# Kernel tuning notes

Hardware: AMD Instinct MI355X
Metric: run time of the kernel (lower is better)

The kernel has to match this reference:

```python
import jax, jax.numpy as jnp
import numpy as np
from jax import lax

B, T, J, C = 256, 512, 25, 3
IN_DIM = J * C  # 75
H = 256


def gru_layer(x, W_ih, W_hh, b_ih, b_hh):
    """PyTorch-semantics GRU layer. x: [B,T,Din] -> (out [B,T,H], h_T [B,H]).
    Gate order in stacked weights: r, z, n (PyTorch convention)."""
    Hh = W_hh.shape[1]
    # precompute input contributions for all timesteps
    xg = jnp.einsum('bti,gi->btg', x, W_ih) + b_ih  # [B,T,3H]

    def step(h, xg_t):
        hg = h @ W_hh.T + b_hh  # [B,3H]
        xr, xz, xn = jnp.split(xg_t, 3, axis=-1)
        hr, hz, hn = jnp.split(hg, 3, axis=-1)
        r = jax.nn.sigmoid(xr + hr)
        z = jax.nn.sigmoid(xz + hz)
        n = jnp.tanh(xn + r * hn)
        h_new = (1.0 - z) * n + z * h
        return h_new, h_new

    h0 = jnp.zeros((x.shape[0], Hh), x.dtype)
    hT, outs = lax.scan(step, h0, jnp.swapaxes(xg, 0, 1))  # scan over time
    return jnp.swapaxes(outs, 0, 1), hT


def setup_inputs() -> dict:
    key = jax.random.key(0)
    ks = jax.random.split(key, 12)
    s_in = 1.0 / np.sqrt(H)

    def u(k, shape):
        return jax.random.uniform(k, shape, jnp.float32, -s_in, s_in)

    return {
        'x': jax.random.normal(ks[0], (B, T, J, C), jnp.float32),
        'W_ih0': u(ks[1], (3 * H, IN_DIM)),
        'W_hh0': u(ks[2], (3 * H, H)),
        'b_ih0': u(ks[3], (3 * H,)),
        'b_hh0': u(ks[4], (3 * H,)),
        'W_ih1': u(ks[5], (3 * H, H)),
        'W_hh1': u(ks[6], (3 * H, H)),
        'b_ih1': u(ks[7], (3 * H,)),
        'b_hh1': u(ks[8], (3 * H,)),
        'fc_W': u(ks[9], (H, H)),
        'fc_b': u(ks[10], (H,)),
    }


def reference(x, W_ih0, W_hh0, b_ih0, b_hh0, W_ih1, W_hh1, b_ih1, b_hh1, fc_W, fc_b):
    b, t, j, c = x.shape
    xf = x.reshape(b, t, j * 3)  # matches torch view(B, T, J*3)
    out0, _ = gru_layer(xf, W_ih0, W_hh0, b_ih0, b_hh0)
    _, hT = gru_layer(out0, W_ih1, W_hh1, b_ih1, b_hh1)
    # unidirectional: final hidden state of last layer -> fc
    embedding = hT @ fc_W.T + fc_b  # [B, H]
    return embedding
```

## Files before the change

kernel.cpp:

```cpp
#include <hip/hip_runtime.h>
#include <hip/hip_bf16.h>
#include <stdint.h>
#include <stddef.h>


typedef _Float16 f16;
typedef _Float16 f16x8 __attribute__((ext_vector_type(8)));
typedef _Float16 f16x4 __attribute__((ext_vector_type(4)));
typedef float    f32x4 __attribute__((ext_vector_type(4)));

#define B_      256
#define T_      512
#define H_      256
#define G_      768
#define IN_RAW  75
#define KX      96
#define MROWS   (T_*B_)

__device__ __forceinline__ float sigm(float x){ return 1.f/(1.f+__expf(-x)); }
__device__ __forceinline__ float tanh_(float x){ return 1.f - 2.f/(1.f+__expf(2.f*x)); }

__global__ __launch_bounds__(256) void cast_x(const float* __restrict__ x,
                                              f16* __restrict__ xb){
  int idx = blockIdx.x*256 + threadIdx.x;
  int row = idx / KX;
  int j   = idx - row*KX;
  int t   = row >> 8;
  int b   = row & 255;
  float v = (j < IN_RAW) ? x[((size_t)b*T_ + t)*IN_RAW + j] : 0.f;
  xb[idx] = (f16)v;
}

__global__ __launch_bounds__(256) void cast_w(
    const float* __restrict__ Wih0, const float* __restrict__ Whh0,
    const float* __restrict__ Wih1, const float* __restrict__ Whh1,
    const float* __restrict__ fcW,
    const float* __restrict__ bih0, const float* __restrict__ bhh0,
    const float* __restrict__ bih1, const float* __restrict__ bhh1,
    f16* __restrict__ W0h, f16* __restrict__ Whh0h, f16* __restrict__ Wih1h,
    f16* __restrict__ Whh1h, f16* __restrict__ fcWh,
    float* __restrict__ bias0, float* __restrict__ bias1){
  int i = blockIdx.x*256 + threadIdx.x;
  if (i < 73728){ int r = i/KX, j = i - r*KX;
    W0h[i] = (f16)((j < IN_RAW) ? Wih0[r*IN_RAW + j] : 0.f); return; }
  i -= 73728;
  if (i < 196608){ Whh0h[i] = (f16)Whh0[i]; return; } i -= 196608;
  if (i < 196608){ Wih1h[i] = (f16)Wih1[i]; return; } i -= 196608;
  if (i < 196608){ Whh1h[i] = (f16)Whh1[i]; return; } i -= 196608;
  if (i < 65536){ fcWh[i] = (f16)fcW[i]; return; } i -= 65536;
  if (i < 768){ bias0[i] = bih0[i] + (i < 512 ? bhh0[i] : 0.f); return; } i -= 768;
  if (i < 768){ bias1[i] = bih1[i] + (i < 512 ? bhh1[i] : 0.f); }
}

__global__ __launch_bounds__(256) void cast_h(const float* __restrict__ hs,
                                              f16* __restrict__ hT){
  int i = blockIdx.x*256 + threadIdx.x;
  hT[i] = (f16)hs[i];
}

template<int K, int BN, bool OUTF32>
__global__ __launch_bounds__(256, 2) void gemm_k(const f16* __restrict__ A,
    const f16* __restrict__ W, const float* __restrict__ bias,
    void* __restrict__ outp, const int N){
  constexpr int NT = BN/16;
  const int tid  = threadIdx.x;
  const int wave = tid >> 6, lane = tid & 63;
  const int quad = lane >> 4, l16 = lane & 15;
  const long mbase = (long)blockIdx.x*128 + wave*32;
  const int  nbase = blockIdx.y*BN;
  f32x4 acc[2][NT] = {};
#pragma unroll 2
  for (int kc = 0; kc < K/32; ++kc){
    f16x8 a0 = *(const f16x8*)(A + (mbase +      l16)*K + kc*32 + quad*8);
    f16x8 a1 = *(const f16x8*)(A + (mbase + 16 + l16)*K + kc*32 + quad*8);
#pragma unroll
    for (int nt = 0; nt < NT; ++nt){
      f16x8 b = *(const f16x8*)(W + (long)(nbase + nt*16 + l16)*K + kc*32 + quad*8);
      acc[0][nt] = __builtin_amdgcn_mfma_f32_16x16x32_f16(a0, b, acc[0][nt], 0, 0, 0);
      acc[1][nt] = __builtin_amdgcn_mfma_f32_16x16x32_f16(a1, b, acc[1][nt], 0, 0, 0);
    }
  }
#pragma unroll
  for (int nt = 0; nt < NT; ++nt){
    const int col = nbase + nt*16 + l16;
    const float bv = bias[col];
#pragma unroll
    for (int af = 0; af < 2; ++af){
#pragma unroll
      for (int r = 0; r < 4; ++r){
        const long row = mbase + af*16 + quad*4 + r;
        float v = acc[af][nt][r] + bv;
        if (OUTF32) ((float*)outp)[row*(long)N + col] = v;
        else        ((f16*)outp)[row*(long)N + col] = (f16)v;
      }
    }
  }
}

template<int K>
__device__ __forceinline__ void gemm_body(const f16* __restrict__ A,
    const f16* __restrict__ W, const float* __restrict__ bias,
    f16* __restrict__ out, const int bx, const int by){
  const int tid  = threadIdx.x;
  const int wave = tid >> 6, lane = tid & 63;
  const int quad = lane >> 4, l16 = lane & 15;
  const int nbase = by*192;
#pragma unroll
  for (int mt = 0; mt < 2; ++mt){
    const long mbase = (long)bx*512 + mt*256 + wave*32;
    f32x4 acc[2][12] = {};
#pragma unroll 2
    for (int kc = 0; kc < K/32; ++kc){
      f16x8 a0 = *(const f16x8*)(A + (mbase +      l16)*K + kc*32 + quad*8);
      f16x8 a1 = *(const f16x8*)(A + (mbase + 16 + l16)*K + kc*32 + quad*8);
#pragma unroll
      for (int nt = 0; nt < 12; ++nt){
        f16x8 b = *(const f16x8*)(W + (long)(nbase + nt*16 + l16)*K + kc*32 + quad*8);
        acc[0][nt] = __builtin_amdgcn_mfma_f32_16x16x32_f16(a0, b, acc[0][nt], 0, 0, 0);
        acc[1][nt] = __builtin_amdgcn_mfma_f32_16x16x32_f16(a1, b, acc[1][nt], 0, 0, 0);
      }
    }
#pragma unroll
    for (int nt = 0; nt < 12; ++nt){
      const int col = nbase + nt*16 + l16;
      const float bv = bias[col];
#pragma unroll
      for (int af = 0; af < 2; ++af)
#pragma unroll
        for (int r = 0; r < 4; ++r)
          out[(mbase + af*16 + quad*4 + r)*(long)G_ + col] = (f16)(acc[af][nt][r] + bv);
    }
  }
}

__device__ __forceinline__ void scan_body(const f16* __restrict__ xg,
    const f16* __restrict__ Whh, const float* __restrict__ bhh,
    float* __restrict__ hstate, f16* __restrict__ out0,
    const int TC, const int bx){
  __shared__ f16   hbuf[2][16*264];
  __shared__ f16   nlds[32768];
  __shared__ float bnlds[256];
  const int tid  = threadIdx.x;
  const int wave = tid >> 6, lane = tid & 63;
  const int quad = lane >> 4, l16 = lane & 15;
  const int b0   = bx*16;
  const int jj   = wave*32 + quad*4;

  f16x8 w[2][2][8];
  f16x8 wn[2][4];
#pragma unroll
  for (int s = 0; s < 2; ++s){
#pragma unroll
    for (int g = 0; g < 2; ++g)
#pragma unroll
      for (int kc = 0; kc < 8; ++kc)
        w[s][g][kc] = *(const f16x8*)(Whh + (size_t)(g*256 + wave*32 + s*16 + l16)*H_ + kc*32 + quad*8);
#pragma unroll
    for (int kc = 0; kc < 4; ++kc)
      wn[s][kc] = *(const f16x8*)(Whh + (size_t)(512 + wave*32 + s*16 + l16)*H_ + kc*32 + quad*8);
  }
#pragma unroll
  for (int s = 0; s < 2; ++s){
#pragma unroll
    for (int g = 0; g < 2; ++g)
#pragma unroll
      for (int kc = 0; kc < 8; ++kc)
        asm volatile("" : "+v"(w[s][g][kc]));
#pragma unroll
    for (int kc = 0; kc < 4; ++kc)
      asm volatile("" : "+v"(wn[s][kc]));
  }

#pragma unroll
  for (int i = 0; i < 8; ++i){
    const int p  = tid*8 + i;
    const int f  = p >> 6, L = p & 63;
    const int wv = f >> 3, ss = (f >> 2) & 1, kcm = f & 3;
    const int row = 512 + wv*32 + ss*16 + (L & 15);
    const int k   = (kcm + 4)*32 + (L >> 4)*8;
    *(f16x8*)&nlds[p*8] = *(const f16x8*)(Whh + (size_t)row*H_ + k);
  }
  if (tid < 256) bnlds[tid] = bhh[512 + tid];

  f32x4 h[2];
#pragma unroll
  for (int s = 0; s < 2; ++s){
    h[s] = *(const f32x4*)(hstate + (size_t)(b0 + l16)*H_ + jj + s*16);
    f16x4 hh;
#pragma unroll
    for (int r = 0; r < 4; ++r) hh[r] = (f16)h[s][r];
    *(f16x4*)&hbuf[0][l16*264 + jj + s*16] = hh;
  }

  const f16* xgl = xg + (size_t)(b0 + l16)*G_ + jj;
  f16x4 cur[6];
#pragma unroll
  for (int s = 0; s < 2; ++s)
#pragma unroll
    for (int g = 0; g < 3; ++g)
      cur[s*3+g] = *(const f16x4*)(xgl + g*256 + s*16);

  __syncthreads();

  for (int t = 0; t < TC; ++t){
    const int pb = t & 1;
    f32x4 acc[2][3] = {};
#pragma unroll
    for (int kc = 0; kc < 8; ++kc){
      f16x8 hf = *(const f16x8*)(&hbuf[pb][l16*264 + kc*32 + quad*8]);
#pragma unroll
      for (int s = 0; s < 2; ++s){
        acc[s][0] = __builtin_amdgcn_mfma_f32_16x16x32_f16(w[s][0][kc], hf, acc[s][0], 0,0,0);
        acc[s][1] = __builtin_amdgcn_mfma_f32_16x16x32_f16(w[s][1][kc], hf, acc[s][1], 0,0,0);
        f16x8 wnf;
        if (kc < 4) wnf = wn[s][kc];
        else        wnf = *(const f16x8*)&nlds[(((wave*2+s)*4 + (kc-4))*64 + lane)*8];
        acc[s][2] = __builtin_amdgcn_mfma_f32_16x16x32_f16(wnf, hf, acc[s][2], 0,0,0);
      }
    }
    f16x4 hh[2];
#pragma unroll
    for (int s = 0; s < 2; ++s){
      const f32x4 bnv = *(const f32x4*)&bnlds[jj + s*16];
#pragma unroll
      for (int r = 0; r < 4; ++r){
        float rg = sigm((float)cur[s*3+0][r] + acc[s][0][r]);
        float zg = sigm((float)cur[s*3+1][r] + acc[s][1][r]);
        float ng = tanh_((float)cur[s*3+2][r] + rg*(acc[s][2][r] + bnv[r]));
        float hv = (1.f - zg)*ng + zg*h[s][r];
        h[s][r] = hv;
        hh[s][r] = (f16)hv;
      }
    }
    if (t+1 < TC){
      const f16* xn_ = xgl + (size_t)(t+1)*(B_*G_);
#pragma unroll
      for (int s = 0; s < 2; ++s)
#pragma unroll
        for (int g = 0; g < 3; ++g)
          cur[s*3+g] = *(const f16x4*)(xn_ + g*256 + s*16);
    }
#pragma unroll
    for (int s = 0; s < 2; ++s){
      *(f16x4*)&hbuf[pb^1][l16*264 + jj + s*16] = hh[s];
      if (out0)
        *(f16x4*)(out0 + ((size_t)t*B_ + b0 + l16)*H_ + jj + s*16) = hh[s];
    }
    __syncthreads();
  }

#pragma unroll
  for (int s = 0; s < 2; ++s)
    *(f32x4*)(hstate + (size_t)(b0 + l16)*H_ + jj + s*16) = h[s];
}

__global__ __launch_bounds__(512, 2) void fused(
    const f16* __restrict__ xg0, const f16* __restrict__ Whh0,
    const float* __restrict__ bhh0, float* __restrict__ h0s,
    f16* __restrict__ out0w,
    const f16* __restrict__ xg1, const f16* __restrict__ Whh1,
    const float* __restrict__ bhh1, float* __restrict__ h1s,
    const f16* __restrict__ g0A, const f16* __restrict__ g0W,
    const float* __restrict__ g0b, f16* __restrict__ g0out,
    const f16* __restrict__ g1A, const f16* __restrict__ g1W,
    const float* __restrict__ g1b, f16* __restrict__ g1out,
    const int TC, const int mask){
  const int bid = blockIdx.x;
  if (bid < 16){
    if (!(mask & 1)) return;
    scan_body(xg0, Whh0, bhh0, h0s, out0w, TC, bid);
  } else if (bid < 32){
    if (!(mask & 2)) return;
    scan_body(xg1, Whh1, bhh1, h1s, (f16*)nullptr, TC, bid - 16);
  } else {
    int g = bid - 32;
    const int half = TC/2;
    if (g < 2*TC){
      if (!(mask & 4)) return;
      gemm_body<96>(g0A, g0W, g0b, g0out, g % half, g / half);
    } else {
      g -= 2*TC;
      if (!(mask & 8)) return;
      gemm_body<256>(g1A, g1W, g1b, g1out, g % half, g / half);
    }
  }
}

extern "C" void kernel_launch(void* const* d_in, const int* in_sizes, int n_in,
                              void* d_out, int out_size, void* d_ws, size_t ws_size,
                              hipStream_t stream){
  (void)in_sizes; (void)n_in; (void)out_size;
  const float* x    = (const float*)d_in[0];
  const float* Wih0 = (const float*)d_in[1];
  const float* Whh0 = (const float*)d_in[2];
  const float* bih0 = (const float*)d_in[3];
  const float* bhh0 = (const float*)d_in[4];
  const float* Wih1 = (const float*)d_in[5];
  const float* Whh1 = (const float*)d_in[6];
  const float* bih1 = (const float*)d_in[7];
  const float* bhh1 = (const float*)d_in[8];
  const float* fcW  = (const float*)d_in[9];
  const float* fcb  = (const float*)d_in[10];

  char* ws = (char*)d_ws;
  size_t off = 0;
  auto alloc = [&](size_t bytes) -> void* {
    void* p = ws + off; off += (bytes + 255) & ~(size_t)255; return p;
  };
  f16*   xb    = (f16*)  alloc((size_t)MROWS*KX*2);
  f16*   W0h   = (f16*)  alloc((size_t)G_*KX*2);
  f16*   Whh0h = (f16*)  alloc((size_t)G_*H_*2);
  f16*   Wih1h = (f16*)  alloc((size_t)G_*H_*2);
  f16*   Whh1h = (f16*)  alloc((size_t)G_*H_*2);
  f16*   fcWh  = (f16*)  alloc((size_t)H_*H_*2);
  float* bias0 = (float*)alloc(G_*4);
  float* bias1 = (float*)alloc(G_*4);
  float* h0s   = (float*)alloc((size_t)B_*H_*4);
  float* h1s   = (float*)alloc((size_t)B_*H_*4);
  f16*   hTh   = (f16*)  alloc((size_t)B_*H_*2);
  const size_t fixed = off;

  int TC = 32;
  while (TC > 8 && fixed + (size_t)TC*1835008 + 1024 > ws_size) TC >>= 1;
  f16* xg0[2], *xg1[2], *out0[2];
  xg0[0]  = (f16*)alloc((size_t)TC*B_*G_*2);
  xg0[1]  = (f16*)alloc((size_t)TC*B_*G_*2);
  xg1[0]  = (f16*)alloc((size_t)TC*B_*G_*2);
  xg1[1]  = (f16*)alloc((size_t)TC*B_*G_*2);
  out0[0] = (f16*)alloc((size_t)TC*B_*H_*2);
  out0[1] = (f16*)alloc((size_t)TC*B_*H_*2);
  const int nc = T_ / TC;

  hipMemsetAsync(h0s, 0, (size_t)B_*H_*4*2, stream);
  hipLaunchKernelGGL(cast_x, dim3(49152), dim3(256), 0, stream, x, xb);
  hipLaunchKernelGGL(cast_w, dim3(2854), dim3(256), 0, stream,
                     Wih0, Whh0, Wih1, Whh1, fcW, bih0, bhh0, bih1, bhh1,
                     W0h, Whh0h, Wih1h, Whh1h, fcWh, bias0, bias1);

  hipLaunchKernelGGL((gemm_k<96,192,false>), dim3(TC*2,4), dim3(256), 0, stream,
                     xb, W0h, bias0, (void*)xg0[0], G_);

  const dim3 grid(32 + 4*TC);
  for (int i = 0; i <= nc + 1; ++i){
    int mask = 0;
    if (i < nc)            mask |= 1;
    if (i >= 2)            mask |= 2;
    if (i + 1 < nc)        mask |= 4;
    if (i >= 1 && i <= nc) mask |= 8;
    hipLaunchKernelGGL(fused, grid, dim3(512), 0, stream,
                       xg0[i&1], Whh0h, bhh0, h0s, out0[i&1],
                       xg1[i&1], Whh1h, bhh1, h1s,
                       xb + (size_t)(i+1)*TC*B_*KX, W0h, bias0, xg0[(i+1)&1],
                       out0[(i+1)&1], Wih1h, bias1, xg1[(i+1)&1],
                       TC, mask);
  }

  hipLaunchKernelGGL(cast_h, dim3(256), dim3(256), 0, stream, h1s, hTh);
  hipLaunchKernelGGL((gemm_k<256,64,true>), dim3(2,4), dim3(256), 0, stream,
                     hTh, fcWh, fcb, d_out, H_);
}
```

Baseline: 1.956 ms.

## Move full n-gate weights to LDS, swizzle h buffer, narrow fused GEMM tiles

The scan now keeps the whole n-gate recurrent weight slice in LDS (128KB) instead of half in registers, and pins the r/z weights in AGPRs. The hidden-state LDS buffer uses an XOR-swizzled layout in place of padding, meant to avoid bank conflicts on the per-step reads. The fused GEMM blocks drop from 192 to 128 output columns, and the grid grows to keep the same coverage with more, smaller blocks. This trades register pressure for more LDS traffic on every timestep and a larger LDS footprint per block.

Measured after the change: 1.917 ms. -2.0%, faster.

```diff
diff --git a/kernel.cpp b/kernel.cpp
--- a/kernel.cpp
+++ b/kernel.cpp
@@ -98,30 +98,30 @@
 }
 
 template<int K>
-__device__ __forceinline__ void gemm_body(const f16* __restrict__ A,
+__device__ __forceinline__ void gemm_body128(const f16* __restrict__ A,
     const f16* __restrict__ W, const float* __restrict__ bias,
     f16* __restrict__ out, const int bx, const int by){
   const int tid  = threadIdx.x;
   const int wave = tid >> 6, lane = tid & 63;
   const int quad = lane >> 4, l16 = lane & 15;
-  const int nbase = by*192;
+  const int nbase = by*128;
 #pragma unroll
   for (int mt = 0; mt < 2; ++mt){
     const long mbase = (long)bx*512 + mt*256 + wave*32;
-    f32x4 acc[2][12] = {};
+    f32x4 acc[2][8] = {};
 #pragma unroll 2
     for (int kc = 0; kc < K/32; ++kc){
       f16x8 a0 = *(const f16x8*)(A + (mbase +      l16)*K + kc*32 + quad*8);
       f16x8 a1 = *(const f16x8*)(A + (mbase + 16 + l16)*K + kc*32 + quad*8);
 #pragma unroll
-      for (int nt = 0; nt < 12; ++nt){
+      for (int nt = 0; nt < 8; ++nt){
         f16x8 b = *(const f16x8*)(W + (long)(nbase + nt*16 + l16)*K + kc*32 + quad*8);
         acc[0][nt] = __builtin_amdgcn_mfma_f32_16x16x32_f16(a0, b, acc[0][nt], 0, 0, 0);
         acc[1][nt] = __builtin_amdgcn_mfma_f32_16x16x32_f16(a1, b, acc[1][nt], 0, 0, 0);
       }
     }
 #pragma unroll
-    for (int nt = 0; nt < 12; ++nt){
+    for (int nt = 0; nt < 8; ++nt){
       const int col = nbase + nt*16 + l16;
       const float bv = bias[col];
 #pragma unroll
@@ -137,8 +137,8 @@
     const f16* __restrict__ Whh, const float* __restrict__ bhh,
     float* __restrict__ hstate, f16* __restrict__ out0,
     const int TC, const int bx){
-  __shared__ f16   hbuf[2][16*264];
-  __shared__ f16   nlds[32768];
+  __shared__ char  hbufB[2][16*512];
+  __shared__ f16   nlds[65536];
   __shared__ float bnlds[256];
   const int tid  = threadIdx.x;
   const int wave = tid >> 6, lane = tid & 63;
@@ -147,38 +147,29 @@
   const int jj   = wave*32 + quad*4;
 
   f16x8 w[2][2][8];
-  f16x8 wn[2][4];
-#pragma unroll
-  for (int s = 0; s < 2; ++s){
+#pragma unroll
+  for (int s = 0; s < 2; ++s)
 #pragma unroll
     for (int g = 0; g < 2; ++g)
 #pragma unroll
       for (int kc = 0; kc < 8; ++kc)
         w[s][g][kc] = *(const f16x8*)(Whh + (size_t)(g*256 + wave*32 + s*16 + l16)*H_ + kc*32 + quad*8);
 #pragma unroll
-    for (int kc = 0; kc < 4; ++kc)
-      wn[s][kc] = *(const f16x8*)(Whh + (size_t)(512 + wave*32 + s*16 + l16)*H_ + kc*32 + quad*8);
-  }
-#pragma unroll
-  for (int s = 0; s < 2; ++s){
+  for (int s = 0; s < 2; ++s)
 #pragma unroll
     for (int g = 0; g < 2; ++g)
 #pragma unroll
       for (int kc = 0; kc < 8; ++kc)
-        asm volatile("" : "+v"(w[s][g][kc]));
-#pragma unroll
-    for (int kc = 0; kc < 4; ++kc)
-      asm volatile("" : "+v"(wn[s][kc]));
-  }
-
-#pragma unroll
-  for (int i = 0; i < 8; ++i){
-    const int p  = tid*8 + i;
+        asm volatile("" : "+a"(w[s][g][kc]));
+
+#pragma unroll
+  for (int i = 0; i < 16; ++i){
+    const int p  = i*512 + tid;
     const int f  = p >> 6, L = p & 63;
-    const int wv = f >> 3, ss = (f >> 2) & 1, kcm = f & 3;
+    const int wv = f >> 4, ss = (f >> 3) & 1, kcc = f & 7;
     const int row = 512 + wv*32 + ss*16 + (L & 15);
-    const int k   = (kcm + 4)*32 + (L >> 4)*8;
-    *(f16x8*)&nlds[p*8] = *(const f16x8*)(Whh + (size_t)row*H_ + k);
+    const int k   = kcc*32 + (L >> 4)*8;
+    *(f16x8*)&nlds[(size_t)p*8] = *(const f16x8*)(Whh + (size_t)row*H_ + k);
   }
   if (tid < 256) bnlds[tid] = bhh[512 + tid];
 
@@ -189,7 +180,8 @@
     f16x4 hh;
 #pragma unroll
     for (int r = 0; r < 4; ++r) hh[r] = (f16)h[s][r];
-    *(f16x4*)&hbuf[0][l16*264 + jj + s*16] = hh;
+    const int ch = wave*4 + s*2 + (quad>>1);
+    *(f16x4*)&hbufB[0][l16*512 + ((ch ^ (l16&7))<<4) + ((quad&1)<<3)] = hh;
   }
 
   const f16* xgl = xg + (size_t)(b0 + l16)*G_ + jj;
@@ -207,15 +199,13 @@
     f32x4 acc[2][3] = {};
 #pragma unroll
     for (int kc = 0; kc < 8; ++kc){
-      f16x8 hf = *(const f16x8*)(&hbuf[pb][l16*264 + kc*32 + quad*8]);
+      f16x8 hf = *(const f16x8*)&hbufB[pb][l16*512 + ((((kc<<2)|quad) ^ (l16&7))<<4)];
 #pragma unroll
       for (int s = 0; s < 2; ++s){
         acc[s][0] = __builtin_amdgcn_mfma_f32_16x16x32_f16(w[s][0][kc], hf, acc[s][0], 0,0,0);
         acc[s][1] = __builtin_amdgcn_mfma_f32_16x16x32_f16(w[s][1][kc], hf, acc[s][1], 0,0,0);
-        f16x8 wnf;
-        if (kc < 4) wnf = wn[s][kc];
-        else        wnf = *(const f16x8*)&nlds[(((wave*2+s)*4 + (kc-4))*64 + lane)*8];
-        acc[s][2] = __builtin_amdgcn_mfma_f32_16x16x32_f16(wnf, hf, acc[s][2], 0,0,0);
+        f16x8 nf = *(const f16x8*)&nlds[(size_t)(((wave<<4)|(s<<3)|kc)*64 + lane)*8];
+        acc[s][2] = __builtin_amdgcn_mfma_f32_16x16x32_f16(nf, hf, acc[s][2], 0,0,0);
       }
     }
     f16x4 hh[2];
@@ -242,7 +232,8 @@
     }
 #pragma unroll
     for (int s = 0; s < 2; ++s){
-      *(f16x4*)&hbuf[pb^1][l16*264 + jj + s*16] = hh[s];
+      const int ch = wave*4 + s*2 + (quad>>1);
+      *(f16x4*)&hbufB[pb^1][l16*512 + ((ch ^ (l16&7))<<4) + ((quad&1)<<3)] = hh[s];
       if (out0)
         *(f16x4*)(out0 + ((size_t)t*B_ + b0 + l16)*H_ + jj + s*16) = hh[s];
     }
@@ -254,7 +245,9 @@
     *(f32x4*)(hstate + (size_t)(b0 + l16)*H_ + jj + s*16) = h[s];
 }
 
-__global__ __launch_bounds__(512, 2) void fused(
+__global__ __launch_bounds__(512)
+__attribute__((amdgpu_waves_per_eu(2, 2)))
+void fused(
     const f16* __restrict__ xg0, const f16* __restrict__ Whh0,
     const float* __restrict__ bhh0, float* __restrict__ h0s,
     f16* __restrict__ out0w,
@@ -274,14 +267,14 @@
     scan_body(xg1, Whh1, bhh1, h1s, (f16*)nullptr, TC, bid - 16);
   } else {
     int g = bid - 32;
-    const int half = TC/2;
-    if (g < 2*TC){
+    const int RB = TC/2;
+    if (g < 3*TC){
       if (!(mask & 4)) return;
-      gemm_body<96>(g0A, g0W, g0b, g0out, g % half, g / half);
+      gemm_body128<96>(g0A, g0W, g0b, g0out, g % RB, g / RB);
     } else {
-      g -= 2*TC;
+      g -= 3*TC;
       if (!(mask & 8)) return;
-      gemm_body<256>(g1A, g1W, g1b, g1out, g % half, g / half);
+      gemm_body128<256>(g1A, g1W, g1b, g1out, g % RB, g / RB);
     }
   }
 }
@@ -340,7 +333,7 @@
   hipLaunchKernelGGL((gemm_k<96,192,false>), dim3(TC*2,4), dim3(256), 0, stream,
                      xb, W0h, bias0, (void*)xg0[0], G_);
 
-  const dim3 grid(32 + 4*TC);
+  const dim3 grid(32 + 6*TC);
   for (int i = 0; i <= nc + 1; ++i){
     int mask = 0;
     if (i < nc)            mask |= 1;
```
